# Kernel optimization log

Hardware: AMD Instinct MI355X
Metric: run time of the kernel (lower is better)

The kernel has to match this reference:

```python
import jax, jax.numpy as jnp
import numpy as np
from jax import lax

B, S, T = 4096, 512, 25


def setup_inputs() -> dict:
    key = jax.random.key(0)
    k1, k2, k3, k4, k5, k6 = jax.random.split(key, 6)
    emissions = jax.random.normal(k1, (B, S, T), dtype=jnp.float32)
    start_transitions = jax.random.normal(k2, (T,), dtype=jnp.float32) * 0.1
    end_transitions = jax.random.normal(k3, (T,), dtype=jnp.float32) * 0.1
    transitions = jax.random.normal(k4, (T, T), dtype=jnp.float32) * 0.1
    labels = jax.random.randint(k5, (B, S), 0, T, dtype=jnp.int32)
    lengths = jax.random.randint(k6, (B,), S // 2, S + 1, dtype=jnp.int32)
    mask = jnp.arange(S, dtype=jnp.int32)[None, :] < lengths[:, None]  # [B,S] bool, mask[:,0]=True
    return {"emissions": emissions, "start_transitions": start_transitions,
            "end_transitions": end_transitions, "transitions": transitions,
            "labels": labels, "mask": mask}


def _crf_llh(emissions, start_transitions, end_transitions, transitions, labels, mask):
    # torchcrf.CRF forward with batch_first=True, reduction='token_mean'
    b, s, t = emissions.shape
    maskf = mask.astype(emissions.dtype)

    # ---- numerator: score of the gold tag sequence ----
    first_tags = labels[:, 0]                                  # [B]
    score = start_transitions[first_tags] + emissions[jnp.arange(b), 0, first_tags]
    trans_scores = transitions[labels[:, :-1], labels[:, 1:]]  # [B,S-1]
    emit_scores = jnp.take_along_axis(emissions, labels[..., None], axis=2)[..., 0]  # [B,S]
    score = score + jnp.sum((trans_scores + emit_scores[:, 1:]) * maskf[:, 1:], axis=1)
    seq_lens = jnp.sum(mask.astype(jnp.int32), axis=1)         # [B]
    last_tags = jnp.take_along_axis(labels, (seq_lens - 1)[:, None], axis=1)[:, 0]
    numerator = score + end_transitions[last_tags]

    # ---- denominator: forward algorithm (log partition) ----
    alpha0 = start_transitions[None, :] + emissions[:, 0]      # [B,T]

    def step(alpha, xs):
        emit_t, mask_t = xs                                    # [B,T], [B]
        # broadcast: alpha[b,i] + transitions[i,j] + emit_t[b,j]
        next_alpha = jax.nn.logsumexp(alpha[:, :, None] + transitions[None, :, :]
                                      + emit_t[:, None, :], axis=1)
        alpha = jnp.where(mask_t[:, None], next_alpha, alpha)
        return alpha, None

    emits = jnp.swapaxes(emissions[:, 1:], 0, 1)               # [S-1,B,T]
    masks = jnp.swapaxes(mask[:, 1:], 0, 1)                    # [S-1,B]
    alpha, _ = lax.scan(step, alpha0, (emits, masks))
    denominator = jax.nn.logsumexp(alpha + end_transitions[None, :], axis=1)  # [B]

    llh = numerator - denominator                              # [B]
    return jnp.sum(llh) / jnp.sum(maskf)                       # token_mean


def reference(emissions, start_transitions, end_transitions, transitions, labels, mask):
    return _crf_llh(emissions, start_transitions, end_transitions, transitions, labels, mask)
```

## Files before the change

kernel.cpp:

```cpp
#include <hip/hip_runtime.h>
#include <stdint.h>

#define TT 25
#define SS 512
#define BB 4096
#define RST 36
#define IL2 1.4426950408889634f
#define LN2F 0.6931471805599453f

__device__ __forceinline__ float ex2(float x){ return __builtin_amdgcn_exp2f(x); }
__device__ __forceinline__ float lg2(float x){ return __builtin_amdgcn_logf(x); }
__device__ __forceinline__ int iclampi(int x,int lo,int hi){ return min(max(x,lo),hi); }

template<int Q>
__device__ __forceinline__ float qb(float v){
  return __int_as_float(__builtin_amdgcn_update_dpp(0, __float_as_int(v), Q*0x55, 0xF, 0xF, true));
}

#define SWZMAX(v,P) v = fmaxf(v, __int_as_float(__builtin_amdgcn_ds_swizzle(__float_as_int(v), P)))
#define SWZADD(v,P) v += __int_as_float(__builtin_amdgcn_ds_swizzle(__float_as_int(v), P))

__device__ __forceinline__ int mask_at(const void* m, int mode, int idx){
  if (mode == 1) return ((const int*)m)[idx] != 0;
  if (mode == 2) return ((const float*)m)[idx] != 0.0f;
  return ((const unsigned char*)m)[idx] != 0;
}

__global__ __launch_bounds__(256, 2)
void crf_main(const float* __restrict__ em, const float* __restrict__ startp,
              const float* __restrict__ endp, const float* __restrict__ transp,
              const int* __restrict__ labels, const void* __restrict__ maskp,
              float* __restrict__ wsr, float* __restrict__ wsl)
{
  __shared__ float smem[16 * RST];
  const int tid  = threadIdx.x;
  const int w    = tid >> 6;
  const int lane = tid & 63;
  const int g    = lane >> 4;
  const int lidx = lane & 15;
  const int dir  = g & 1;
  const int rsel = g >> 1;
  const int row  = blockIdx.x * 8 + w * 2 + rsel;
  const int rbS  = row * SS;
  const int rowbase = (w * 4 + g) * RST;

  const int c1 = 2 * lidx, c2 = 2 * lidx + 1;
  const bool v1 = (c1 < TT), v2 = (c2 < TT);
  const int c1c = v1 ? c1 : (TT - 1), c2c = v2 ? c2 : (TT - 1);
  const int ws2 = (lidx <= 12) ? 2 * lidx : (26 + 2 * (lidx - 13));

  const uint32_t w0 = ((const uint32_t*)maskp)[0];
  const int mode = (w0 == 1u) ? 1 : ((w0 == 0x3F800000u) ? 2 : 0);

  int lens[2];
  const int base2row = blockIdx.x * 8 + w * 2;
#pragma unroll
  for (int r = 0; r < 2; ++r) {
    int mb = (base2row + r) * SS;
    int pq1 = mask_at(maskp, mode, mb + lane * 8);
    unsigned long long b1 = __ballot(pq1);
    int q = __popcll(b1);
    int bs = 8 * (q - 1);
    int pq2 = mask_at(maskp, mode, mb + bs + (lane & 7));
    unsigned long long b2 = __ballot((lane < 8) && pq2);
    lens[r] = bs + __popcll(b2);
  }
  const int L = rsel ? lens[1] : lens[0];
  const int m = (L - 1) >> 1;
  const int iters = dir ? (L - 1 - m) : m;
  const int it0 = lens[0] - 1 - ((lens[0] - 1) >> 1);
  const int it1 = lens[1] - 1 - ((lens[1] - 1) >> 1);
  const int maxIters = max(it0, it1);

  float E1[TT], E2[TT];
#pragma unroll
  for (int i = 0; i < TT; ++i) {
    float t1 = dir ? transp[c1c * TT + i] : transp[i * TT + c1c];
    float t2 = dir ? transp[c2c * TT + i] : transp[i * TT + c2c];
    E1[i] = v1 ? ex2(t1 * IL2) : 0.f;
    E2[i] = v2 ? ex2(t2 * IL2) : 0.f;
  }

  float pf1 = startp[c1c] + em[(size_t)rbS * TT + c1c];
  float pf2 = startp[c2c] + em[(size_t)rbS * TT + c2c];
  float p1 = v1 ? ex2((dir ? endp[c1c] : pf1) * IL2) : 0.f;
  float p2 = v2 ? ex2((dir ? endp[c2c] : pf2) * IL2) : 0.f;

  const int l0 = labels[rbS];
  const int lE = labels[rbS + L - 1];
  float num = dir ? endp[lE] : (startp[l0] + em[(size_t)rbS * TT + l0]);
  int C2 = 0;
  int carry = dir ? lE : l0;

  float emv1[8], emv2[8], tadd[8];
  int labv[8];
#pragma unroll
  for (int u = 0; u < 8; ++u) {
    int t = dir ? (L - 1 - u) : (1 + u);
    t = iclampi(t, 1, L - 1);
    size_t eb = (size_t)(rbS + t) * TT;
    emv1[u] = em[eb + c1c];
    emv2[u] = em[eb + c2c];
    int ni = dir ? (L - 2 - u) : (1 + u);
    ni = iclampi(ni, 0, L - 1);
    int nl = labels[rbS + ni];
    int aL = dir ? nl : carry, bL = dir ? carry : nl;
    tadd[u] = transp[aL * TT + bL] + em[eb + bL];
    carry = nl;
  }
#pragma unroll
  for (int u = 0; u < 8; ++u) {
    int ni = dir ? (L - 2 - (u + 8)) : (1 + u + 8);
    ni = iclampi(ni, 0, L - 1);
    labv[u] = labels[rbS + ni];
  }

  int ubase = 0;

#define STEP(u, FILL)                                                         \
  {                                                                           \
    const int uu = ubase + (u);                                               \
    float e1 = ex2(emv1[u] * IL2), e2 = ex2(emv2[u] * IL2);                   \
    float ta = tadd[u];                                                       \
    bool live = uu < iters;                                                   \
    num += live ? ta : 0.f;                                                   \
    if (FILL) {                                                               \
      int vf = uu + 8;                                                        \
      int t = dir ? (L - 1 - vf) : (1 + vf);                                  \
      t = iclampi(t, 1, L - 1);                                               \
      size_t eb = (size_t)(rbS + t) * TT;                                     \
      emv1[u] = em[eb + c1c];                                                 \
      emv2[u] = em[eb + c2c];                                                 \
      int nl = labv[u];                                                       \
      int aL = dir ? nl : carry, bL = dir ? carry : nl;                       \
      tadd[u] = transp[aL * TT + bL] + em[eb + bL];                           \
      int ni = dir ? (L - 2 - (vf + 8)) : (1 + vf + 8);                       \
      ni = iclampi(ni, 0, L - 1);                                             \
      labv[u] = labels[rbS + ni];                                             \
      carry = nl;                                                             \
    }                                                                         \
    float w1 = dir ? p1 * e1 : p1, w2v = dir ? p2 * e2 : p2;                  \
    ((float2*)smem)[(rowbase + ws2) >> 1] = make_float2(w1, w2v);             \
    const float4* rp = (const float4*)&smem[rowbase + ((lane & 3) << 3)];     \
    float4 x0 = rp[0], x1 = rp[1];                                            \
    float d1a = 0.f, d1b = 0.f, d2a = 0.f, d2b = 0.f, pv;                     \
    pv = qb<0>(x0.x); d1a = fmaf(pv, E1[0],  d1a); d2a = fmaf(pv, E2[0],  d2a); \
    pv = qb<0>(x0.y); d1b = fmaf(pv, E1[1],  d1b); d2b = fmaf(pv, E2[1],  d2b); \
    pv = qb<0>(x0.z); d1a = fmaf(pv, E1[2],  d1a); d2a = fmaf(pv, E2[2],  d2a); \
    pv = qb<0>(x0.w); d1b = fmaf(pv, E1[3],  d1b); d2b = fmaf(pv, E2[3],  d2b); \
    pv = qb<0>(x1.x); d1a = fmaf(pv, E1[4],  d1a); d2a = fmaf(pv, E2[4],  d2a); \
    pv = qb<0>(x1.y); d1b = fmaf(pv, E1[5],  d1b); d2b = fmaf(pv, E2[5],  d2b); \
    pv = qb<0>(x1.z); d1a = fmaf(pv, E1[6],  d1a); d2a = fmaf(pv, E2[6],  d2a); \
    pv = qb<0>(x1.w); d1b = fmaf(pv, E1[7],  d1b); d2b = fmaf(pv, E2[7],  d2b); \
    pv = qb<1>(x0.x); d1a = fmaf(pv, E1[8],  d1a); d2a = fmaf(pv, E2[8],  d2a); \
    pv = qb<1>(x0.y); d1b = fmaf(pv, E1[9],  d1b); d2b = fmaf(pv, E2[9],  d2b); \
    pv = qb<1>(x0.z); d1a = fmaf(pv, E1[10], d1a); d2a = fmaf(pv, E2[10], d2a); \
    pv = qb<1>(x0.w); d1b = fmaf(pv, E1[11], d1b); d2b = fmaf(pv, E2[11], d2b); \
    pv = qb<1>(x1.x); d1a = fmaf(pv, E1[12], d1a); d2a = fmaf(pv, E2[12], d2a); \
    pv = qb<1>(x1.y); d1b = fmaf(pv, E1[13], d1b); d2b = fmaf(pv, E2[13], d2b); \
    pv = qb<1>(x1.z); d1a = fmaf(pv, E1[14], d1a); d2a = fmaf(pv, E2[14], d2a); \
    pv = qb<1>(x1.w); d1b = fmaf(pv, E1[15], d1b); d2b = fmaf(pv, E2[15], d2b); \
    pv = qb<2>(x0.x); d1a = fmaf(pv, E1[16], d1a); d2a = fmaf(pv, E2[16], d2a); \
    pv = qb<2>(x0.y); d1b = fmaf(pv, E1[17], d1b); d2b = fmaf(pv, E2[17], d2b); \
    pv = qb<2>(x0.z); d1a = fmaf(pv, E1[18], d1a); d2a = fmaf(pv, E2[18], d2a); \
    pv = qb<2>(x0.w); d1b = fmaf(pv, E1[19], d1b); d2b = fmaf(pv, E2[19], d2b); \
    pv = qb<2>(x1.x); d1a = fmaf(pv, E1[20], d1a); d2a = fmaf(pv, E2[20], d2a); \
    pv = qb<2>(x1.y); d1b = fmaf(pv, E1[21], d1b); d2b = fmaf(pv, E2[21], d2b); \
    pv = qb<2>(x1.z); d1a = fmaf(pv, E1[22], d1a); d2a = fmaf(pv, E2[22], d2a); \
    pv = qb<2>(x1.w); d1b = fmaf(pv, E1[23], d1b); d2b = fmaf(pv, E2[23], d2b); \
    pv = qb<3>(x0.x); d1a = fmaf(pv, E1[24], d1a); d2a = fmaf(pv, E2[24], d2a); \
    float d1 = d1a + d1b, d2 = d2a + d2b;                                     \
    float p1n = dir ? d1 : d1 * e1, p2n = dir ? d2 : d2 * e2;                 \
    p1 = live ? p1n : p1; p2 = live ? p2n : p2;                               \
  }

#define RESCALE {                                                             \
    float mx = fmaxf(p1, p2);                                                 \
    SWZMAX(mx, 0x041F); SWZMAX(mx, 0x081F);                                   \
    SWZMAX(mx, 0x101F); SWZMAX(mx, 0x201F);                                   \
    int ef = (__float_as_int(mx) >> 23) & 0xFF;                               \
    C2 += ef - 127;                                                           \
    float sc = __int_as_float((254 - ef) << 23);                              \
    p1 *= sc; p2 *= sc; }

  for (; ubase + 8 <= maxIters; ubase += 8) {
    STEP(0, 1) STEP(1, 1) STEP(2, 1) STEP(3, 1)
    STEP(4, 1) STEP(5, 1) STEP(6, 1) STEP(7, 1)
    RESCALE
  }
  {
    int rem = maxIters - ubase;
    if (rem > 0) STEP(0, 0)
    if (rem > 1) STEP(1, 0)
    if (rem > 2) STEP(2, 0)
    if (rem > 3) STEP(3, 0)
    if (rem > 4) STEP(4, 0)
    if (rem > 5) STEP(5, 0)
    if (rem > 6) STEP(6, 0)
  }
  RESCALE

#undef STEP
#undef RESCALE

  ((float2*)smem)[(rowbase + ws2) >> 1] = make_float2(p1, p2);
  smem[rowbase + 32] = num;
  smem[rowbase + 33] = __int_as_float(C2);
  const int pbase = (w * 4 + (g ^ 1)) * RST;
  float2 qq = ((float2*)smem)[(pbase + ws2) >> 1];
  float prod = p1 * qq.x + p2 * qq.y;
  SWZADD(prod, 0x041F); SWZADD(prod, 0x081F);
  SWZADD(prod, 0x101F); SWZADD(prod, 0x201F);
  float onum = smem[pbase + 32];
  int oC2 = __float_as_int(smem[pbase + 33]);
  if (lidx == 0 && dir == 0) {
    float den = LN2F * (lg2(prod) + (float)(C2 + oC2));
    wsr[row] = (num + onum) - den;
    wsl[row] = (float)L;
  }
}

__global__ void crf_reduce(const float* __restrict__ wsr,
                           const float* __restrict__ wsl,
                           float* __restrict__ out)
{
  __shared__ float sr[256], sl[256];
  int t = threadIdx.x;
  float a = 0.0f, c = 0.0f;
  for (int i = t; i < BB; i += 256) { a += wsr[i]; c += wsl[i]; }
  sr[t] = a; sl[t] = c;
  __syncthreads();
  for (int k = 128; k > 0; k >>= 1) {
    if (t < k) { sr[t] += sr[t + k]; sl[t] += sl[t + k]; }
    __syncthreads();
  }
  if (t == 0) out[0] = sr[0] / sl[0];
}

extern "C" void kernel_launch(void* const* d_in, const int* in_sizes, int n_in,
                              void* d_out, int out_size, void* d_ws, size_t ws_size,
                              hipStream_t stream)
{
  const float* em = (const float*)d_in[0];
  const float* st = (const float*)d_in[1];
  const float* en = (const float*)d_in[2];
  const float* tr = (const float*)d_in[3];
  const int*   lb = (const int*)d_in[4];
  const void*  mk = d_in[5];
  float* wsr = (float*)d_ws;
  float* wsl = wsr + BB;
  crf_main<<<BB / 8, 256, 0, stream>>>(em, st, en, tr, lb, mk, wsr, wsl);
  crf_reduce<<<1, 256, 0, stream>>>(wsr, wsl, (float*)d_out);
}
```

Baseline: 116.9 us.

## Replace LDS broadcast matvec with DPP row-rotate across 16-lane group

The per-step matrix-vector product no longer writes the alpha vector to shared memory and reads it back with quad broadcasts. Each lane now rotates its own pair of values through the 16-lane DPP row using row_ror, and the exponentiated transition coefficients are pre-permuted per lane to match the rotation order. This removes an LDS store/load round trip from the serial recurrence. In exchange it adds more DPP ops per step (15 rotations on two values) and more per-lane coefficient registers.

Measured after the change: 174.6 us. 49.4% more time.

```diff
diff --git a/kernel.cpp b/kernel.cpp
--- a/kernel.cpp
+++ b/kernel.cpp
@@ -12,9 +12,11 @@
 __device__ __forceinline__ float lg2(float x){ return __builtin_amdgcn_logf(x); }
 __device__ __forceinline__ int iclampi(int x,int lo,int hi){ return min(max(x,lo),hi); }
 
-template<int Q>
-__device__ __forceinline__ float qb(float v){
-  return __int_as_float(__builtin_amdgcn_update_dpp(0, __float_as_int(v), Q*0x55, 0xF, 0xF, true));
+template<int K>
+__device__ __forceinline__ float rotk(float v){
+  if constexpr (K == 0) return v;
+  else return __int_as_float(__builtin_amdgcn_update_dpp(
+      0, __float_as_int(v), 0x120 | K, 0xF, 0xF, true));
 }
 
 #define SWZMAX(v,P) v = fmaxf(v, __int_as_float(__builtin_amdgcn_ds_swizzle(__float_as_int(v), P)))
@@ -72,13 +74,21 @@
   const int it1 = lens[1] - 1 - ((lens[1] - 1) >> 1);
   const int maxIters = max(it0, it1);
 
-  float E1[TT], E2[TT];
-#pragma unroll
-  for (int i = 0; i < TT; ++i) {
-    float t1 = dir ? transp[c1c * TT + i] : transp[i * TT + c1c];
-    float t2 = dir ? transp[c2c * TT + i] : transp[i * TT + c2c];
-    E1[i] = v1 ? ex2(t1 * IL2) : 0.f;
-    E2[i] = v2 ? ex2(t2 * IL2) : 0.f;
+  float Ea1[16], Eb1[16], Ea2[16], Eb2[16];
+#pragma unroll
+  for (int k = 0; k < 16; ++k) {
+    int s  = (lidx - k) & 15;
+    int i1 = 2 * s, i2 = 2 * s + 1;
+    bool q1 = (i1 < TT), q2 = (i2 < TT);
+    int i1c = q1 ? i1 : 0, i2c = q2 ? i2 : 0;
+    float t11 = dir ? transp[c1c * TT + i1c] : transp[i1c * TT + c1c];
+    float t21 = dir ? transp[c1c * TT + i2c] : transp[i2c * TT + c1c];
+    float t12 = dir ? transp[c2c * TT + i1c] : transp[i1c * TT + c2c];
+    float t22 = dir ? transp[c2c * TT + i2c] : transp[i2c * TT + c2c];
+    Ea1[k] = (q1 && v1) ? ex2(t11 * IL2) : 0.f;
+    Eb1[k] = (q2 && v1) ? ex2(t21 * IL2) : 0.f;
+    Ea2[k] = (q1 && v2) ? ex2(t12 * IL2) : 0.f;
+    Eb2[k] = (q2 && v2) ? ex2(t22 * IL2) : 0.f;
   }
 
   float pf1 = startp[c1c] + em[(size_t)rbS * TT + c1c];
@@ -116,6 +126,11 @@
   }
 
   int ubase = 0;
+
+#define ROTK(K)                                                               \
+    { float r1 = rotk<K>(w1), r2 = rotk<K>(w2v);                              \
+      d1a = fmaf(r1, Ea1[K], d1a); d1b = fmaf(r2, Eb1[K], d1b);               \
+      d2a = fmaf(r1, Ea2[K], d2a); d2b = fmaf(r2, Eb2[K], d2b); }
 
 #define STEP(u, FILL)                                                         \
   {                                                                           \
@@ -140,35 +155,11 @@
       carry = nl;                                                             \
     }                                                                         \
     float w1 = dir ? p1 * e1 : p1, w2v = dir ? p2 * e2 : p2;                  \
-    ((float2*)smem)[(rowbase + ws2) >> 1] = make_float2(w1, w2v);             \
-    const float4* rp = (const float4*)&smem[rowbase + ((lane & 3) << 3)];     \
-    float4 x0 = rp[0], x1 = rp[1];                                            \
-    float d1a = 0.f, d1b = 0.f, d2a = 0.f, d2b = 0.f, pv;                     \
-    pv = qb<0>(x0.x); d1a = fmaf(pv, E1[0],  d1a); d2a = fmaf(pv, E2[0],  d2a); \
-    pv = qb<0>(x0.y); d1b = fmaf(pv, E1[1],  d1b); d2b = fmaf(pv, E2[1],  d2b); \
-    pv = qb<0>(x0.z); d1a = fmaf(pv, E1[2],  d1a); d2a = fmaf(pv, E2[2],  d2a); \
-    pv = qb<0>(x0.w); d1b = fmaf(pv, E1[3],  d1b); d2b = fmaf(pv, E2[3],  d2b); \
-    pv = qb<0>(x1.x); d1a = fmaf(pv, E1[4],  d1a); d2a = fmaf(pv, E2[4],  d2a); \
-    pv = qb<0>(x1.y); d1b = fmaf(pv, E1[5],  d1b); d2b = fmaf(pv, E2[5],  d2b); \
-    pv = qb<0>(x1.z); d1a = fmaf(pv, E1[6],  d1a); d2a = fmaf(pv, E2[6],  d2a); \
-    pv = qb<0>(x1.w); d1b = fmaf(pv, E1[7],  d1b); d2b = fmaf(pv, E2[7],  d2b); \
-    pv = qb<1>(x0.x); d1a = fmaf(pv, E1[8],  d1a); d2a = fmaf(pv, E2[8],  d2a); \
-    pv = qb<1>(x0.y); d1b = fmaf(pv, E1[9],  d1b); d2b = fmaf(pv, E2[9],  d2b); \
-    pv = qb<1>(x0.z); d1a = fmaf(pv, E1[10], d1a); d2a = fmaf(pv, E2[10], d2a); \
-    pv = qb<1>(x0.w); d1b = fmaf(pv, E1[11], d1b); d2b = fmaf(pv, E2[11], d2b); \
-    pv = qb<1>(x1.x); d1a = fmaf(pv, E1[12], d1a); d2a = fmaf(pv, E2[12], d2a); \
-    pv = qb<1>(x1.y); d1b = fmaf(pv, E1[13], d1b); d2b = fmaf(pv, E2[13], d2b); \
-    pv = qb<1>(x1.z); d1a = fmaf(pv, E1[14], d1a); d2a = fmaf(pv, E2[14], d2a); \
-    pv = qb<1>(x1.w); d1b = fmaf(pv, E1[15], d1b); d2b = fmaf(pv, E2[15], d2b); \
-    pv = qb<2>(x0.x); d1a = fmaf(pv, E1[16], d1a); d2a = fmaf(pv, E2[16], d2a); \
-    pv = qb<2>(x0.y); d1b = fmaf(pv, E1[17], d1b); d2b = fmaf(pv, E2[17], d2b); \
-    pv = qb<2>(x0.z); d1a = fmaf(pv, E1[18], d1a); d2a = fmaf(pv, E2[18], d2a); \
-    pv = qb<2>(x0.w); d1b = fmaf(pv, E1[19], d1b); d2b = fmaf(pv, E2[19], d2b); \
-    pv = qb<2>(x1.x); d1a = fmaf(pv, E1[20], d1a); d2a = fmaf(pv, E2[20], d2a); \
-    pv = qb<2>(x1.y); d1b = fmaf(pv, E1[21], d1b); d2b = fmaf(pv, E2[21], d2b); \
-    pv = qb<2>(x1.z); d1a = fmaf(pv, E1[22], d1a); d2a = fmaf(pv, E2[22], d2a); \
-    pv = qb<2>(x1.w); d1b = fmaf(pv, E1[23], d1b); d2b = fmaf(pv, E2[23], d2b); \
-    pv = qb<3>(x0.x); d1a = fmaf(pv, E1[24], d1a); d2a = fmaf(pv, E2[24], d2a); \
+    float d1a = 0.f, d1b = 0.f, d2a = 0.f, d2b = 0.f;                         \
+    ROTK(0)  ROTK(1)  ROTK(2)  ROTK(3)                                        \
+    ROTK(4)  ROTK(5)  ROTK(6)  ROTK(7)                                        \
+    ROTK(8)  ROTK(9)  ROTK(10) ROTK(11)                                       \
+    ROTK(12) ROTK(13) ROTK(14) ROTK(15)                                       \
     float d1 = d1a + d1b, d2 = d2a + d2b;                                     \
     float p1n = dir ? d1 : d1 * e1, p2n = dir ? d2 : d2 * e2;                 \
     p1 = live ? p1n : p1; p2 = live ? p2n : p2;                               \
@@ -201,6 +192,7 @@
   RESCALE
 
 #undef STEP
+#undef ROTK
 #undef RESCALE
 
   ((float2*)smem)[(rowbase + ws2) >> 1] = make_float2(p1, p2);
```
